# Optimization experiments

Measured on AMD Instinct MI355X. Metric: run time of the kernel, lower is better.

## Reference

```python
import jax, jax.numpy as jnp
import numpy as np

NHEADS = 2
STRENGTH = 0.1
ZED = 8  # zone_embed_dim
STATE_DIM = 137
HID = 256
NBLOCKS = 4
BATCH = 131072


def _mha_seq1(q, k, v, in_w, in_b, out_w, out_b):
    """nn.MultiheadAttention (batch_first) with q,k,v of shape [B,1,E]."""
    B, _, E = q.shape
    hd = E // NHEADS
    Wq, Wk, Wv = in_w[:E], in_w[E:2 * E], in_w[2 * E:]
    bq, bk, bv = in_b[:E], in_b[E:2 * E], in_b[2 * E:]

    def heads(x, W, b):
        return (x @ W.T + b).reshape(B, -1, NHEADS, hd).transpose(0, 2, 1, 3)  # [B,H,1,hd]

    qh, kh, vh = heads(q, Wq, bq), heads(k, Wk, bk), heads(v, Wv, bv)
    scale = 1.0 / jnp.sqrt(jnp.asarray(hd, q.dtype))
    s = jnp.einsum('bhqd,bhkd->bhqk', qh, kh) * scale
    a = jax.nn.softmax(s, axis=-1)  # trivially ones for kv_len=1, kept for fidelity
    o = jnp.einsum('bhqk,bhkd->bhqd', a, vh).transpose(0, 2, 1, 3).reshape(B, -1, E)
    return o @ out_w.T + out_b


def setup_inputs() -> dict:
    key = jax.random.key(0)
    ks = jax.random.split(key, 20)
    S, H, N = STATE_DIM, HID, NBLOCKS
    ahd = S - ZED - 1  # 128

    def w(k, shape, fan_in):
        return jax.random.normal(k, shape, jnp.float32) * (1.0 / np.sqrt(fan_in))

    inp = {
        't': jax.random.uniform(ks[0], (1,), jnp.float32) * 24.0,
        'state': jax.random.normal(ks[1], (BATCH, S), jnp.float32),
        'W0': w(ks[2], (H, S + 2), S + 2), 'b0': jnp.zeros((H,), jnp.float32),
        'blkW1': w(ks[3], (N, H, H), H), 'blkb1': jnp.zeros((N, H), jnp.float32),
        'blkW2': w(ks[4], (N, H, H), H), 'blkb2': jnp.zeros((N, H), jnp.float32),
        'Wout': w(ks[5], (S, H), H), 'bout': jnp.zeros((S,), jnp.float32),
        'lm_in_w': w(ks[6], (3 * ZED, ZED), ZED), 'lm_in_b': jnp.zeros((3 * ZED,), jnp.float32),
        'lm_out_w': w(ks[7], (ZED, ZED), ZED), 'lm_out_b': jnp.zeros((ZED,), jnp.float32),
        'ta_in_w': w(ks[8], (3 * ahd, ahd), ahd), 'ta_in_b': jnp.zeros((3 * ahd,), jnp.float32),
        'ta_out_w': w(ks[9], (ahd, ahd), ahd), 'ta_out_b': jnp.zeros((ahd,), jnp.float32),
    }
    return inp


def reference(t, state, W0, b0, blkW1, blkb1, blkW2, blkb2, Wout, bout,
              lm_in_w, lm_in_b, lm_out_w, lm_out_b,
              ta_in_w, ta_in_b, ta_out_w, ta_out_b):
    B, S = state.shape
    ahd = S - ZED - 1
    two_pi_over_24 = 2.0 * jnp.pi / 24.0
    tv = jnp.concatenate([jnp.sin(t * two_pi_over_24), jnp.cos(t * two_pi_over_24)])  # [2]
    t_vec = jnp.broadcast_to(tv, (B, 2))

    # core dynamics MLP: Linear -> ReLU -> residual blocks -> Linear
    x = jnp.concatenate([state, t_vec], axis=-1)
    h = jax.nn.relu(x @ W0.T + b0)
    for i in range(blkW1.shape[0]):
        inner = jnp.tanh(h @ blkW1[i].T + blkb1[i]) @ blkW2[i].T + blkb2[i]
        h = jnp.tanh(h + inner)
    core = h @ Wout.T + bout

    # attention delta
    hs = state[:, :ahd]
    loc = state[:, ahd:ahd + ZED]
    mov = state[:, -1:]

    q_lm = jnp.broadcast_to(mov, (B, ZED))[:, None, :]
    loc_e = loc[:, None, :]
    enh_loc = _mha_seq1(q_lm, loc_e, loc_e, lm_in_w, lm_in_b, lm_out_w, lm_out_b)[:, 0]
    delta_loc = enh_loc - loc

    t_pad = jnp.concatenate([t_vec, jnp.zeros((B, ahd - 2), state.dtype)], axis=-1)[:, None, :]
    h_e = hs[:, None, :]
    enh_h = _mha_seq1(t_pad, h_e, h_e, ta_in_w, ta_in_b, ta_out_w, ta_out_b)[:, 0]
    delta_h = enh_h - hs

    delta = jnp.concatenate([delta_h, delta_loc, jnp.zeros_like(mov)], axis=-1)
    return core + STRENGTH * delta
```

## Files before the change

kernel.cpp:

```cpp
#include <hip/hip_runtime.h>

typedef __attribute__((ext_vector_type(8))) short short8;
typedef __attribute__((ext_vector_type(4))) float float4_;

#define SDIM    137
#define HID     256
#define K0PAD   160
#define KAUG    416
#define MTILE   128
#define NROWT   (MTILE / 16)
#define NTHR    512

struct __attribute__((aligned(8))) U2 { unsigned x, y; };

__device__ __forceinline__ unsigned short f2bf(float f) {
  union { float f; unsigned int i; } v; v.f = f;
  return (unsigned short)((v.i + 0x8000u) >> 16);
}
__device__ __forceinline__ unsigned pack_bf16(float a, float b) {
  union { float f; unsigned u; } ua, ub; ua.f = a; ub.f = b;
  return __builtin_amdgcn_perm(ub.u + 0x8000u, ua.u + 0x8000u, 0x07060302u);
}
__device__ __forceinline__ float lo_bf(unsigned p) {
  union { unsigned u; float f; } v; v.u = p << 16; return v.f;
}
__device__ __forceinline__ float hi_bf(unsigned p) {
  union { unsigned u; float f; } v; v.u = p & 0xFFFF0000u; return v.f;
}
__device__ __forceinline__ float fast_tanh(float x) {
  float e = __expf(2.f * x);
  float r = __builtin_amdgcn_rcpf(e + 1.f);
  return __builtin_fmaf(-2.f, r, 1.f);
}
__device__ __forceinline__ int sidx(int row, int col) {
  return row * 256 + ((((col >> 3) ^ (row & 31)) << 3) | (col & 7));
}

template<int NK, int LDB, int BOFF>
__device__ __forceinline__ void mma_wact(const unsigned short* __restrict__ X,
                                         const unsigned short* __restrict__ W,
                                         float4_ (&acc)[2][NROWT], int lane, int colbase)
{
  const int q  = lane >> 4;
  const int rm = lane & 15;
  short8 wa[NK][2];
  #pragma unroll
  for (int kb = 0; kb < NK; ++kb)
    #pragma unroll
    for (int mt = 0; mt < 2; ++mt) {
      int m = colbase + mt * 16 + rm;
      wa[kb][mt] = *(const short8*)(W + (size_t)m * LDB + BOFF + kb * 32 + q * 8);
    }
  #pragma unroll
  for (int kb = 0; kb < NK; ++kb) {
    short8 xb[NROWT];
    #pragma unroll
    for (int nt = 0; nt < NROWT; ++nt) {
      int row = nt * 16 + rm;
      int c   = kb * 4 + q;
      xb[nt] = *(const short8*)(X + row * 256 + (((c ^ (row & 31)) << 3)));
    }
    #pragma unroll
    for (int mt = 0; mt < 2; ++mt)
      #pragma unroll
      for (int nt = 0; nt < NROWT; ++nt)
        acc[mt][nt] = __builtin_amdgcn_mfma_f32_16x16x32_bf16(wa[kb][mt], xb[nt], acc[mt][nt], 0, 0, 0);
  }
}


__global__ void prep_w0(const float* __restrict__ t,
                        const float* __restrict__ W0,
                        const float* __restrict__ b0,
                        unsigned short* __restrict__ W0p,
                        float* __restrict__ b0p)
{
  int n = blockIdx.x;
  int tt = threadIdx.x;
  for (int k = tt; k < K0PAD; k += 64)
    W0p[n * K0PAD + k] = (k < SDIM) ? f2bf(W0[n * 139 + k]) : (unsigned short)0;
  if (tt == 0) {
    float tv  = t[0];
    float ang = tv * (6.2831853071795864f / 24.0f);
    float sv = __sinf(ang), cv = __cosf(ang);
    b0p[n] = b0[n] + W0[n * 139 + 137] * sv + W0[n * 139 + 138] * cv;
  }
}

__global__ void prep_fill(const float* __restrict__ Wout,
                          const float* __restrict__ bout,
                          unsigned short* __restrict__ Waug,
                          float* __restrict__ baug)
{
  int n = blockIdx.x;
  int tt = threadIdx.x;
  if (tt < KAUG / 4) {
    int k0 = tt * 4;
    U2 p;
    if (k0 < 256 && n < SDIM) {
      float4_ v = *(const float4_*)(Wout + (size_t)n * 256 + k0);
      p.x = pack_bf16(v[0], v[1]); p.y = pack_bf16(v[2], v[3]);
    } else {
      p.x = 0u; p.y = 0u;
    }
    *(U2*)(Waug + (size_t)n * KAUG + k0) = p;
  } else if (tt == KAUG / 4) {
    baug[n] = (n < SDIM) ? bout[n] : 0.f;
  }
}

__global__ void prep_ta(const float* __restrict__ ta_in_w,
                        const float* __restrict__ ta_in_b,
                        const float* __restrict__ ta_out_w,
                        const float* __restrict__ ta_out_b,
                        const float* __restrict__ lm_in_w,
                        const float* __restrict__ lm_in_b,
                        const float* __restrict__ lm_out_w,
                        const float* __restrict__ lm_out_b,
                        unsigned short* __restrict__ Waug,
                        float* __restrict__ baug)
{
  __shared__ float red[128];
  int blk = blockIdx.x;
  int tt  = threadIdx.x;
  if (blk < 128) {
    int n = blk, s = tt;
    float dot = 0.f;
    #pragma unroll 8
    for (int r = 0; r < 128; ++r)
      dot += ta_out_w[n * 128 + r] * ta_in_w[(256 + r) * 128 + s];
    float v = 0.1f * (dot - (s == n ? 1.f : 0.f));
    Waug[(size_t)n * KAUG + 256 + s] = f2bf(v);

    red[tt] = ta_out_w[n * 128 + tt] * ta_in_b[256 + tt];
    __syncthreads();
    if (tt < 64) {
      float p = red[tt] + red[tt + 64];
      for (int off = 32; off; off >>= 1) p += __shfl_down(p, off);
      if (tt == 0) baug[n] += 0.1f * (p + ta_out_b[n]);
    }
  } else {
    if (tt < 64) {
      int a = tt >> 3, b = tt & 7;
      float dot = 0.f;
      #pragma unroll
      for (int r = 0; r < 8; ++r)
        dot += lm_out_w[a * 8 + r] * lm_in_w[(16 + r) * 8 + b];
      Waug[(size_t)(128 + a) * KAUG + 384 + b] = f2bf(0.1f * (dot - (a == b ? 1.f : 0.f)));
    } else if (tt < 72) {
      int a = tt - 64;
      float dot = 0.f;
      #pragma unroll
      for (int r = 0; r < 8; ++r)
        dot += lm_out_w[a * 8 + r] * lm_in_b[16 + r];
      baug[128 + a] += 0.1f * (dot + lm_out_b[a]);
    }
  }
}

__global__ void prep_blk2(const float* __restrict__ s1, const float* __restrict__ s2,
                          unsigned short* __restrict__ d1, unsigned short* __restrict__ d2)
{
  int i = (blockIdx.x * 256 + threadIdx.x) * 4;
  const float* s; unsigned short* d;
  if (i < 262144) { s = s1 + i;          d = d1 + i; }
  else            { s = s2 + i - 262144; d = d2 + i - 262144; }
  float4_ v = *(const float4_*)s;
  U2 p; p.x = pack_bf16(v[0], v[1]); p.y = pack_bf16(v[2], v[3]);
  *(U2*)d = p;
}


__global__ __launch_bounds__(NTHR, 2)
void fused_odefunc(
    const float* __restrict__ state,
    const unsigned short* __restrict__ W0p,
    const float* __restrict__ b0p,
    const unsigned short* __restrict__ blkW1,
    const float* __restrict__ blkb1,
    const unsigned short* __restrict__ blkW2,
    const float* __restrict__ blkb2,
    const unsigned short* __restrict__ Waug,
    const float* __restrict__ baug,
    float* __restrict__ out)
{
  __shared__ __align__(16) unsigned short ARENA[2 * MTILE * 256];
  unsigned short* H = ARENA;
  unsigned short* G = ARENA + MTILE * 256;
  float*          T = (float*)ARENA;

  const int tid  = threadIdx.x;
  const int lane = tid & 63;
  const int wave = tid >> 6;
  const int q    = lane >> 4;
  const int rm   = lane & 15;
  const int cb   = wave * 32;
  const int row0 = blockIdx.x * MTILE;

  #pragma unroll 2
  for (int qd = tid; qd < MTILE * (K0PAD / 4); qd += NTHR) {
    int m  = qd / (K0PAD / 4);
    int k0 = (qd - m * (K0PAD / 4)) * 4;
    const float* sp = state + (size_t)(row0 + m) * SDIM + k0;
    float f0 = (k0     < SDIM) ? sp[0] : 0.f;
    float f1 = (k0 + 1 < SDIM) ? sp[1] : 0.f;
    float f2 = (k0 + 2 < SDIM) ? sp[2] : 0.f;
    float f3 = (k0 + 3 < SDIM) ? sp[3] : 0.f;
    U2 p; p.x = pack_bf16(f0, f1); p.y = pack_bf16(f2, f3);
    *(U2*)(&G[sidx(m, k0)]) = p;
  }
  __syncthreads();

  {
    float4_ acc[2][NROWT];
    #pragma unroll
    for (int mt = 0; mt < 2; ++mt)
      #pragma unroll
      for (int nt = 0; nt < NROWT; ++nt) acc[mt][nt] = (float4_){0.f, 0.f, 0.f, 0.f};
    mma_wact<K0PAD / 32, K0PAD, 0>(G, W0p, acc, lane, cb);
    #pragma unroll
    for (int mt = 0; mt < 2; ++mt) {
      int col0 = cb + mt * 16 + q * 4;
      float4_ bias = *(const float4_*)(b0p + col0);
      #pragma unroll
      for (int nt = 0; nt < NROWT; ++nt) {
        int row = nt * 16 + rm;
        float v0 = fmaxf(acc[mt][nt][0] + bias[0], 0.f);
        float v1 = fmaxf(acc[mt][nt][1] + bias[1], 0.f);
        float v2 = fmaxf(acc[mt][nt][2] + bias[2], 0.f);
        float v3 = fmaxf(acc[mt][nt][3] + bias[3], 0.f);
        U2 p; p.x = pack_bf16(v0, v1); p.y = pack_bf16(v2, v3);
        *(U2*)(&H[sidx(row, col0)]) = p;
      }
    }
  }
  __syncthreads();

  for (int blk = 0; blk < 4; ++blk) {
    const unsigned short* W1 = blkW1 + (size_t)blk * 65536;
    const float*          b1 = blkb1 + blk * 256;
    const unsigned short* W2 = blkW2 + (size_t)blk * 65536;
    const float*          b2 = blkb2 + blk * 256;

    float4_ acc[2][NROWT];
    #pragma unroll
    for (int mt = 0; mt < 2; ++mt)
      #pragma unroll
      for (int nt = 0; nt < NROWT; ++nt) acc[mt][nt] = (float4_){0.f, 0.f, 0.f, 0.f};
    mma_wact<8, 256, 0>(H, W1, acc, lane, cb);
    #pragma unroll
    for (int mt = 0; mt < 2; ++mt) {
      int col0 = cb + mt * 16 + q * 4;
      float4_ bias = *(const float4_*)(b1 + col0);
      #pragma unroll
      for (int nt = 0; nt < NROWT; ++nt) {
        int row = nt * 16 + rm;
        float v0 = fast_tanh(acc[mt][nt][0] + bias[0]);
        float v1 = fast_tanh(acc[mt][nt][1] + bias[1]);
        float v2 = fast_tanh(acc[mt][nt][2] + bias[2]);
        float v3 = fast_tanh(acc[mt][nt][3] + bias[3]);
        U2 p; p.x = pack_bf16(v0, v1); p.y = pack_bf16(v2, v3);
        *(U2*)(&G[sidx(row, col0)]) = p;
      }
    }
    __syncthreads();

    #pragma unroll
    for (int mt = 0; mt < 2; ++mt)
      #pragma unroll
      for (int nt = 0; nt < NROWT; ++nt) acc[mt][nt] = (float4_){0.f, 0.f, 0.f, 0.f};
    mma_wact<8, 256, 0>(G, W2, acc, lane, cb);
    #pragma unroll
    for (int mt = 0; mt < 2; ++mt) {
      int col0 = cb + mt * 16 + q * 4;
      float4_ bias = *(const float4_*)(b2 + col0);
      #pragma unroll
      for (int nt = 0; nt < NROWT; ++nt) {
        int row = nt * 16 + rm;
        int idx = sidx(row, col0);
        U2 old = *(const U2*)(&H[idx]);
        float v0 = fast_tanh(lo_bf(old.x) + acc[mt][nt][0] + bias[0]);
        float v1 = fast_tanh(hi_bf(old.x) + acc[mt][nt][1] + bias[1]);
        float v2 = fast_tanh(lo_bf(old.y) + acc[mt][nt][2] + bias[2]);
        float v3 = fast_tanh(hi_bf(old.y) + acc[mt][nt][3] + bias[3]);
        U2 p; p.x = pack_bf16(v0, v1); p.y = pack_bf16(v2, v3);
        *(U2*)(&H[idx]) = p;
      }
    }
    __syncthreads();
  }

  #pragma unroll 2
  for (int qd = tid; qd < MTILE * (K0PAD / 4); qd += NTHR) {
    int m  = qd / (K0PAD / 4);
    int k0 = (qd - m * (K0PAD / 4)) * 4;
    const float* sp = state + (size_t)(row0 + m) * SDIM + k0;
    float f0 = (k0     < SDIM) ? sp[0] : 0.f;
    float f1 = (k0 + 1 < SDIM) ? sp[1] : 0.f;
    float f2 = (k0 + 2 < SDIM) ? sp[2] : 0.f;
    float f3 = (k0 + 3 < SDIM) ? sp[3] : 0.f;
    U2 p; p.x = pack_bf16(f0, f1); p.y = pack_bf16(f2, f3);
    *(U2*)(&G[sidx(m, k0)]) = p;
  }

  float4_ acc[2][NROWT];
  #pragma unroll
  for (int mt = 0; mt < 2; ++mt)
    #pragma unroll
    for (int nt = 0; nt < NROWT; ++nt) acc[mt][nt] = (float4_){0.f, 0.f, 0.f, 0.f};
  if (cb < 160)
    mma_wact<8, KAUG, 0>(H, Waug, acc, lane, cb);
  __syncthreads();
  if (cb < 160)
    mma_wact<5, KAUG, 256>(G, Waug, acc, lane, cb);
  __syncthreads();
  if (cb < 160) {
    #pragma unroll
    for (int mt = 0; mt < 2; ++mt) {
      int col0 = cb + mt * 16 + q * 4;
      if (col0 <= 136) {
        float4_ bias = *(const float4_*)(baug + col0);
        #pragma unroll
        for (int nt = 0; nt < NROWT; ++nt) {
          int row = nt * 16 + rm;
          float4_ v;
          v[0] = acc[mt][nt][0] + bias[0];
          v[1] = acc[mt][nt][1] + bias[1];
          v[2] = acc[mt][nt][2] + bias[2];
          v[3] = acc[mt][nt][3] + bias[3];
          *(float4_*)(T + row * 140 + col0) = v;
        }
      }
    }
  }
  __syncthreads();

  float* obase = out + (size_t)row0 * SDIM;
  int r = tid / SDIM;
  int c = tid - r * SDIM;
  #pragma unroll 1
  for (int idx = tid; idx < MTILE * SDIM; idx += NTHR) {
    obase[idx] = T[r * 140 + c];
    c += NTHR - 3 * SDIM;
    r += 3;
    if (c >= SDIM) { c -= SDIM; r += 1; }
  }
}

extern "C" void kernel_launch(void* const* d_in, const int* in_sizes, int n_in,
                              void* d_out, int out_size, void* d_ws, size_t ws_size,
                              hipStream_t stream) {
  const float* t        = (const float*)d_in[0];
  const float* state    = (const float*)d_in[1];
  const float* W0       = (const float*)d_in[2];
  const float* b0       = (const float*)d_in[3];
  const float* blkW1    = (const float*)d_in[4];
  const float* blkb1    = (const float*)d_in[5];
  const float* blkW2    = (const float*)d_in[6];
  const float* blkb2    = (const float*)d_in[7];
  const float* Wout     = (const float*)d_in[8];
  const float* bout     = (const float*)d_in[9];
  const float* lm_in_w  = (const float*)d_in[10];
  const float* lm_in_b  = (const float*)d_in[11];
  const float* lm_out_w = (const float*)d_in[12];
  const float* lm_out_b = (const float*)d_in[13];
  const float* ta_in_w  = (const float*)d_in[14];
  const float* ta_in_b  = (const float*)d_in[15];
  const float* ta_out_w = (const float*)d_in[16];
  const float* ta_out_b = (const float*)d_in[17];

  char* ws = (char*)d_ws;
  unsigned short* W0p   = (unsigned short*)ws;
  float*          b0p   = (float*)(ws + 81920);
  unsigned short* Waug  = (unsigned short*)(ws + 82944);
  float*          baug  = (float*)(ws + 295936);
  unsigned short* W1b   = (unsigned short*)(ws + 296960);
  unsigned short* W2b   = (unsigned short*)(ws + 821248);

  prep_w0<<<256, 64, 0, stream>>>(t, W0, b0, W0p, b0p);
  prep_fill<<<256, 128, 0, stream>>>(Wout, bout, Waug, baug);
  prep_ta<<<129, 128, 0, stream>>>(ta_in_w, ta_in_b, ta_out_w, ta_out_b,
                                   lm_in_w, lm_in_b, lm_out_w, lm_out_b, Waug, baug);
  prep_blk2<<<512, 256, 0, stream>>>(blkW1, blkW2, W1b, W2b);

  int batch = in_sizes[1] / SDIM;
  fused_odefunc<<<batch / MTILE, NTHR, 0, stream>>>(
      state, W0p, b0p, W1b, blkb1, W2b, blkb2, Waug, baug,
      (float*)d_out);
}
```

Before: 496.0 us.

## Fold tanh scale into weights, use exp2, hardware bf16 pack, interleave epilogues

Stores activations pre-scaled by 2/ln2, so tanh becomes exp2 + rcp + fma with no extra multiply. The scale is folded into W0, b0, the biases and Wout (which gets the inverse). It also swaps the manual bf16 packing for the v_cvt_pk_bf16_f32 instruction. The GEMMs are restructured to loop over row tiles, with each tile's epilogue issued right after the next tile's MFMAs so transcendental work overlaps matrix work. It pins waves_per_eu to 2. Scaled bf16 storage changes rounding slightly, and the hidden values now range up to about ±2.885.

```diff
diff --git a/kernel.cpp b/kernel.cpp
--- a/kernel.cpp
+++ b/kernel.cpp
@@ -11,6 +11,9 @@
 #define NROWT   (MTILE / 16)
 #define NTHR    512
 
+#define SCLF 2.8853900817779268f
+#define ISCL 0.34657359027997264f
+
 struct __attribute__((aligned(8))) U2 { unsigned x, y; };
 
 __device__ __forceinline__ unsigned short f2bf(float f) {
@@ -21,19 +24,66 @@
   union { float f; unsigned u; } ua, ub; ua.f = a; ub.f = b;
   return __builtin_amdgcn_perm(ub.u + 0x8000u, ua.u + 0x8000u, 0x07060302u);
 }
+__device__ __forceinline__ unsigned cvt_pk(float a, float b) {
+  unsigned r;
+  asm("v_cvt_pk_bf16_f32 %0, %1, %2" : "=v"(r) : "v"(a), "v"(b));
+  return r;
+}
 __device__ __forceinline__ float lo_bf(unsigned p) {
   union { unsigned u; float f; } v; v.u = p << 16; return v.f;
 }
 __device__ __forceinline__ float hi_bf(unsigned p) {
   union { unsigned u; float f; } v; v.u = p & 0xFFFF0000u; return v.f;
 }
-__device__ __forceinline__ float fast_tanh(float x) {
-  float e = __expf(2.f * x);
+__device__ __forceinline__ float stanh(float y) {
+#if __has_builtin(__builtin_amdgcn_exp2f)
+  float e = __builtin_amdgcn_exp2f(y);
+#else
+  float e = __expf(y * 0.6931471805599453f);
+#endif
   float r = __builtin_amdgcn_rcpf(e + 1.f);
-  return __builtin_fmaf(-2.f, r, 1.f);
+  return __builtin_fmaf(-2.f * SCLF, r, SCLF);
 }
 __device__ __forceinline__ int sidx(int row, int col) {
   return row * 256 + ((((col >> 3) ^ (row & 31)) << 3) | (col & 7));
+}
+__device__ __forceinline__ short8 ld_x(const unsigned short* __restrict__ X, int row, int c) {
+  return *(const short8*)(X + row * 256 + (((c ^ (row & 31)) << 3)));
+}
+
+template<int NK, int LDB, int BOFF>
+__device__ __forceinline__ void load_wa(const unsigned short* __restrict__ W,
+                                        short8 (&wa)[NK][2], int colbase, int rm, int q)
+{
+  #pragma unroll
+  for (int kb = 0; kb < NK; ++kb)
+    #pragma unroll
+    for (int mt = 0; mt < 2; ++mt)
+      wa[kb][mt] = *(const short8*)(W + (size_t)(colbase + mt * 16 + rm) * LDB
+                                      + BOFF + kb * 32 + q * 8);
+}
+
+template<int NK, class EPI>
+__device__ __forceinline__ void gemm_f(const unsigned short* __restrict__ X,
+                                       const short8 (&wa)[NK][2],
+                                       int rm, int q, EPI epi)
+{
+  float4_ a[NROWT][2];
+  #pragma unroll
+  for (int nt = 0; nt < NROWT; ++nt) {
+    short8 xb[NK];
+    #pragma unroll
+    for (int kb = 0; kb < NK; ++kb) xb[kb] = ld_x(X, nt * 16 + rm, kb * 4 + q);
+    a[nt][0] = (float4_){0.f, 0.f, 0.f, 0.f};
+    a[nt][1] = (float4_){0.f, 0.f, 0.f, 0.f};
+    #pragma unroll
+    for (int kb = 0; kb < NK; ++kb) {
+      a[nt][0] = __builtin_amdgcn_mfma_f32_16x16x32_bf16(wa[kb][0], xb[kb], a[nt][0], 0, 0, 0);
+      a[nt][1] = __builtin_amdgcn_mfma_f32_16x16x32_bf16(wa[kb][1], xb[kb], a[nt][1], 0, 0, 0);
+    }
+    if (nt > 0) epi(nt - 1, a[nt - 1]);
+  }
+  epi(NROWT - 1, a[NROWT - 1]);
 }
 
 template<int NK, int LDB, int BOFF>
@@ -44,22 +94,13 @@
   const int q  = lane >> 4;
   const int rm = lane & 15;
   short8 wa[NK][2];
-  #pragma unroll
-  for (int kb = 0; kb < NK; ++kb)
-    #pragma unroll
-    for (int mt = 0; mt < 2; ++mt) {
-      int m = colbase + mt * 16 + rm;
-      wa[kb][mt] = *(const short8*)(W + (size_t)m * LDB + BOFF + kb * 32 + q * 8);
-    }
+  load_wa<NK, LDB, BOFF>(W, wa, colbase, rm, q);
   #pragma unroll
   for (int kb = 0; kb < NK; ++kb) {
     short8 xb[NROWT];
     #pragma unroll
-    for (int nt = 0; nt < NROWT; ++nt) {
-      int row = nt * 16 + rm;
-      int c   = kb * 4 + q;
-      xb[nt] = *(const short8*)(X + row * 256 + (((c ^ (row & 31)) << 3)));
-    }
+    for (int nt = 0; nt < NROWT; ++nt)
+      xb[nt] = ld_x(X, nt * 16 + rm, kb * 4 + q);
     #pragma unroll
     for (int mt = 0; mt < 2; ++mt)
       #pragma unroll
@@ -78,12 +119,12 @@
   int n = blockIdx.x;
   int tt = threadIdx.x;
   for (int k = tt; k < K0PAD; k += 64)
-    W0p[n * K0PAD + k] = (k < SDIM) ? f2bf(W0[n * 139 + k]) : (unsigned short)0;
+    W0p[n * K0PAD + k] = (k < SDIM) ? f2bf(W0[n * 139 + k] * SCLF) : (unsigned short)0;
   if (tt == 0) {
     float tv  = t[0];
     float ang = tv * (6.2831853071795864f / 24.0f);
     float sv = __sinf(ang), cv = __cosf(ang);
-    b0p[n] = b0[n] + W0[n * 139 + 137] * sv + W0[n * 139 + 138] * cv;
+    b0p[n] = SCLF * (b0[n] + W0[n * 139 + 137] * sv + W0[n * 139 + 138] * cv);
   }
 }
 
@@ -99,7 +140,7 @@
     U2 p;
     if (k0 < 256 && n < SDIM) {
       float4_ v = *(const float4_*)(Wout + (size_t)n * 256 + k0);
-      p.x = pack_bf16(v[0], v[1]); p.y = pack_bf16(v[2], v[3]);
+      p.x = pack_bf16(v[0] * ISCL, v[1] * ISCL); p.y = pack_bf16(v[2] * ISCL, v[3] * ISCL);
     } else {
       p.x = 0u; p.y = 0u;
     }
@@ -172,6 +213,7 @@
 
 
 __global__ __launch_bounds__(NTHR, 2)
+__attribute__((amdgpu_waves_per_eu(2, 2)))
 void fused_odefunc(
     const float* __restrict__ state,
     const unsigned short* __restrict__ W0p,
@@ -206,33 +248,30 @@
     float f1 = (k0 + 1 < SDIM) ? sp[1] : 0.f;
     float f2 = (k0 + 2 < SDIM) ? sp[2] : 0.f;
     float f3 = (k0 + 3 < SDIM) ? sp[3] : 0.f;
-    U2 p; p.x = pack_bf16(f0, f1); p.y = pack_bf16(f2, f3);
+    U2 p; p.x = cvt_pk(f0, f1); p.y = cvt_pk(f2, f3);
     *(U2*)(&G[sidx(m, k0)]) = p;
   }
   __syncthreads();
 
   {
-    float4_ acc[2][NROWT];
-    #pragma unroll
-    for (int mt = 0; mt < 2; ++mt)
-      #pragma unroll
-      for (int nt = 0; nt < NROWT; ++nt) acc[mt][nt] = (float4_){0.f, 0.f, 0.f, 0.f};
-    mma_wact<K0PAD / 32, K0PAD, 0>(G, W0p, acc, lane, cb);
-    #pragma unroll
-    for (int mt = 0; mt < 2; ++mt) {
-      int col0 = cb + mt * 16 + q * 4;
-      float4_ bias = *(const float4_*)(b0p + col0);
-      #pragma unroll
-      for (int nt = 0; nt < NROWT; ++nt) {
-        int row = nt * 16 + rm;
-        float v0 = fmaxf(acc[mt][nt][0] + bias[0], 0.f);
-        float v1 = fmaxf(acc[mt][nt][1] + bias[1], 0.f);
-        float v2 = fmaxf(acc[mt][nt][2] + bias[2], 0.f);
-        float v3 = fmaxf(acc[mt][nt][3] + bias[3], 0.f);
-        U2 p; p.x = pack_bf16(v0, v1); p.y = pack_bf16(v2, v3);
+    short8 wa[K0PAD / 32][2];
+    load_wa<K0PAD / 32, K0PAD, 0>(W0p, wa, cb, rm, q);
+    float4_ bias[2];
+    #pragma unroll
+    for (int mt = 0; mt < 2; ++mt) bias[mt] = *(const float4_*)(b0p + cb + mt * 16 + q * 4);
+    gemm_f<K0PAD / 32>(G, wa, rm, q, [&](int nt, float4_ (&a2)[2]) {
+      int row = nt * 16 + rm;
+      #pragma unroll
+      for (int mt = 0; mt < 2; ++mt) {
+        int col0 = cb + mt * 16 + q * 4;
+        float v0 = fmaxf(a2[mt][0] + bias[mt][0], 0.f);
+        float v1 = fmaxf(a2[mt][1] + bias[mt][1], 0.f);
+        float v2 = fmaxf(a2[mt][2] + bias[mt][2], 0.f);
+        float v3 = fmaxf(a2[mt][3] + bias[mt][3], 0.f);
+        U2 p; p.x = cvt_pk(v0, v1); p.y = cvt_pk(v2, v3);
         *(U2*)(&H[sidx(row, col0)]) = p;
       }
-    }
+    });
   }
   __syncthreads();
 
@@ -242,50 +281,57 @@
     const unsigned short* W2 = blkW2 + (size_t)blk * 65536;
     const float*          b2 = blkb2 + blk * 256;
 
-    float4_ acc[2][NROWT];
-    #pragma unroll
-    for (int mt = 0; mt < 2; ++mt)
-      #pragma unroll
-      for (int nt = 0; nt < NROWT; ++nt) acc[mt][nt] = (float4_){0.f, 0.f, 0.f, 0.f};
-    mma_wact<8, 256, 0>(H, W1, acc, lane, cb);
-    #pragma unroll
-    for (int mt = 0; mt < 2; ++mt) {
-      int col0 = cb + mt * 16 + q * 4;
-      float4_ bias = *(const float4_*)(b1 + col0);
-      #pragma unroll
-      for (int nt = 0; nt < NROWT; ++nt) {
+    {
+      short8 wa[8][2];
+      load_wa<8, 256, 0>(W1, wa, cb, rm, q);
+      float4_ bb[2];
+      #pragma unroll
+      for (int mt = 0; mt < 2; ++mt) {
+        float4_ t4 = *(const float4_*)(b1 + cb + mt * 16 + q * 4);
+        bb[mt][0] = t4[0] * SCLF; bb[mt][1] = t4[1] * SCLF;
+        bb[mt][2] = t4[2] * SCLF; bb[mt][3] = t4[3] * SCLF;
+      }
+      gemm_f<8>(H, wa, rm, q, [&](int nt, float4_ (&a2)[2]) {
         int row = nt * 16 + rm;
-        float v0 = fast_tanh(acc[mt][nt][0] + bias[0]);
-        float v1 = fast_tanh(acc[mt][nt][1] + bias[1]);
-        float v2 = fast_tanh(acc[mt][nt][2] + bias[2]);
-        float v3 = fast_tanh(acc[mt][nt][3] + bias[3]);
-        U2 p; p.x = pack_bf16(v0, v1); p.y = pack_bf16(v2, v3);
-        *(U2*)(&G[sidx(row, col0)]) = p;
+        #pragma unroll
+        for (int mt = 0; mt < 2; ++mt) {
+          int col0 = cb + mt * 16 + q * 4;
+          float g0 = stanh(a2[mt][0] + bb[mt][0]);
+          float g1 = stanh(a2[mt][1] + bb[mt][1]);
+          float g2 = stanh(a2[mt][2] + bb[mt][2]);
+          float g3 = stanh(a2[mt][3] + bb[mt][3]);
+          U2 p; p.x = cvt_pk(g0, g1); p.y = cvt_pk(g2, g3);
+          *(U2*)(&G[sidx(row, col0)]) = p;
+        }
+      });
+    }
+    __syncthreads();
+
+    {
+      short8 wa[8][2];
+      load_wa<8, 256, 0>(W2, wa, cb, rm, q);
+      float4_ bb[2];
+      #pragma unroll
+      for (int mt = 0; mt < 2; ++mt) {
+        float4_ t4 = *(const float4_*)(b2 + cb + mt * 16 + q * 4);
+        bb[mt][0] = t4[0] * SCLF; bb[mt][1] = t4[1] * SCLF;
+        bb[mt][2] = t4[2] * SCLF; bb[mt][3] = t4[3] * SCLF;
       }
-    }
-    __syncthreads();
-
-    #pragma unroll
-    for (int mt = 0; mt < 2; ++mt)
-      #pragma unroll
-      for (int nt = 0; nt < NROWT; ++nt) acc[mt][nt] = (float4_){0.f, 0.f, 0.f, 0.f};
-    mma_wact<8, 256, 0>(G, W2, acc, lane, cb);
-    #pragma unroll
-    for (int mt = 0; mt < 2; ++mt) {
-      int col0 = cb + mt * 16 + q * 4;
-      float4_ bias = *(const float4_*)(b2 + col0);
-      #pragma unroll
-      for (int nt = 0; nt < NROWT; ++nt) {
+      gemm_f<8>(G, wa, rm, q, [&](int nt, float4_ (&a2)[2]) {
         int row = nt * 16 + rm;
-        int idx = sidx(row, col0);
-        U2 old = *(const U2*)(&H[idx]);
-        float v0 = fast_tanh(lo_bf(old.x) + acc[mt][nt][0] + bias[0]);
-        float v1 = fast_tanh(hi_bf(old.x) + acc[mt][nt][1] + bias[1]);
-        float v2 = fast_tanh(lo_bf(old.y) + acc[mt][nt][2] + bias[2]);
-        float v3 = fast_tanh(hi_bf(old.y) + acc[mt][nt][3] + bias[3]);
-        U2 p; p.x = pack_bf16(v0, v1); p.y = pack_bf16(v2, v3);
-        *(U2*)(&H[idx]) = p;
-      }
+        #pragma unroll
+        for (int mt = 0; mt < 2; ++mt) {
+          int col0 = cb + mt * 16 + q * 4;
+          int idx = sidx(row, col0);
+          U2 old = *(const U2*)(&H[idx]);
+          float h0 = stanh(lo_bf(old.x) + a2[mt][0] + bb[mt][0]);
+          float h1 = stanh(hi_bf(old.x) + a2[mt][1] + bb[mt][1]);
+          float h2 = stanh(lo_bf(old.y) + a2[mt][2] + bb[mt][2]);
+          float h3 = stanh(hi_bf(old.y) + a2[mt][3] + bb[mt][3]);
+          U2 p; p.x = cvt_pk(h0, h1); p.y = cvt_pk(h2, h3);
+          *(U2*)(&H[idx]) = p;
+        }
+      });
     }
     __syncthreads();
   }
@@ -299,7 +345,7 @@
     float f1 = (k0 + 1 < SDIM) ? sp[1] : 0.f;
     float f2 = (k0 + 2 < SDIM) ? sp[2] : 0.f;
     float f3 = (k0 + 3 < SDIM) ? sp[3] : 0.f;
-    U2 p; p.x = pack_bf16(f0, f1); p.y = pack_bf16(f2, f3);
+    U2 p; p.x = cvt_pk(f0, f1); p.y = cvt_pk(f2, f3);
     *(U2*)(&G[sidx(m, k0)]) = p;
   }
 
```

New measurement: 456.6 us. 1.09x faster.
